# Performance work log

Hardware: AMD Instinct MI355X
Metric: run time of the kernel (lower is better)

## Reference

```python
import jax, jax.numpy as jnp
import numpy as np

NUM_EMBEDDINGS = 512
EMBEDDING_DIM = 64
COMMITMENT_SCALAR = 0.25


def setup_inputs() -> dict:
    key = jax.random.key(0)
    k_in, k_emb = jax.random.split(key)
    inputs = jax.random.normal(k_in, (64, 4096, EMBEDDING_DIM), dtype=jnp.float32)
    # nn.Embedding weight, init U(-1/K, 1/K) as in the torch module
    emb_weight = jax.random.uniform(
        k_emb, (NUM_EMBEDDINGS, EMBEDDING_DIM), dtype=jnp.float32,
        minval=-1.0 / NUM_EMBEDDINGS, maxval=1.0 / NUM_EMBEDDINGS)
    return {"inputs": inputs, "emb_weight": emb_weight}


def reference(inputs, emb_weight):
    input_shape = inputs.shape
    flat = inputs.reshape(-1, EMBEDDING_DIM)  # [N, D]
    distances = (jnp.sum(flat ** 2, axis=1, keepdims=True)
                 + jnp.sum(emb_weight ** 2, axis=1)
                 - 2.0 * flat @ emb_weight.T)
    encoding_indices = jnp.argmin(distances, axis=1)  # [N]
    # one-hot @ codebook == gather of codebook rows
    quantized = emb_weight[encoding_indices].reshape(input_shape)
    e_latent_loss = jnp.mean((jax.lax.stop_gradient(quantized) - inputs) ** 2)
    q_latent_loss = jnp.mean((quantized - jax.lax.stop_gradient(inputs)) ** 2)
    loss = q_latent_loss + COMMITMENT_SCALAR * e_latent_loss
    # straight-through estimator (training mode)
    quantized = inputs + jax.lax.stop_gradient(quantized - inputs)
    return encoding_indices[:, None], quantized, loss
```

## Files before the change

kernel.cpp:

```cpp
#include <hip/hip_runtime.h>


#define NROWS (64 * 4096)
#define DIMS 64
#define KCODES 512
#define BLOCK 256
#define GRID (NROWS / BLOCK)
#define WS_S2_OFF 0
#define WS_RED_OFF 4096

typedef unsigned int u16v __attribute__((ext_vector_type(16)));

__device__ __forceinline__ float pairwise64_sq(const float4* v) {
  float a[64];
  #pragma unroll
  for (int c = 0; c < 16; ++c) {
    a[4 * c + 0] = v[c].x * v[c].x;
    a[4 * c + 1] = v[c].y * v[c].y;
    a[4 * c + 2] = v[c].z * v[c].z;
    a[4 * c + 3] = v[c].w * v[c].w;
  }
  float r0 = a[0], r1 = a[1], r2 = a[2], r3 = a[3];
  float r4 = a[4], r5 = a[5], r6 = a[6], r7 = a[7];
  #pragma unroll
  for (int i = 8; i < 64; i += 8) {
    r0 += a[i + 0]; r1 += a[i + 1]; r2 += a[i + 2]; r3 += a[i + 3];
    r4 += a[i + 4]; r5 += a[i + 5]; r6 += a[i + 6]; r7 += a[i + 7];
  }
  return ((r0 + r1) + (r2 + r3)) + ((r4 + r5) + (r6 + r7));
}

__global__ void vq_s2(const float* __restrict__ emb, float* __restrict__ s2) {
  int k = blockIdx.x * 256 + threadIdx.x;
  const float4* row = (const float4*)(emb + (size_t)k * DIMS);
  float4 r[16];
  #pragma unroll
  for (int c = 0; c < 16; ++c) r[c] = row[c];
  s2[k] = pairwise64_sq(r);
}

#define FMA4(E, j0, c)                                        \
  acc = fmaf(xv[c].x, __uint_as_float(E[(j0) + 0]), acc);     \
  acc = fmaf(xv[c].y, __uint_as_float(E[(j0) + 1]), acc);     \
  acc = fmaf(xv[c].z, __uint_as_float(E[(j0) + 2]), acc);     \
  acc = fmaf(xv[c].w, __uint_as_float(E[(j0) + 3]), acc);

__global__ __launch_bounds__(BLOCK, 4) void vq_main(
    const float* __restrict__ x, const float* __restrict__ emb,
    const float* __restrict__ s2, float* __restrict__ out_idx,
    float* __restrict__ out_q, double* __restrict__ ws) {
  __shared__ int   kidx[BLOCK];
  __shared__ double red[BLOCK / 64];
  const int tid = threadIdx.x;
  const int row0 = blockIdx.x * BLOCK;
  const int r = row0 + tid;

  float4 xv[16];
  {
    const float4* p = (const float4*)(x + (size_t)r * DIMS);
    #pragma unroll
    for (int c = 0; c < 16; ++c) xv[c] = p[c];
  }
  const float s1 = pairwise64_sq(xv);

  float d1 = 3.4e38f;
  int kbest = 0;
  #pragma unroll 1
  for (int k = 0; k < KCODES; ++k) {
    const float* pe = emb + (size_t)k * DIMS;
    const float* ps = s2 + k;
    u16v e0, e1, e2, e3;
    unsigned int bku;
    asm volatile(
        "s_load_dwordx16 %0, %5, 0x0\n\t"
        "s_load_dwordx16 %1, %5, 0x40\n\t"
        "s_load_dwordx16 %2, %5, 0x80\n\t"
        "s_load_dwordx16 %3, %5, 0xc0\n\t"
        "s_load_dword    %4, %6, 0x0\n\t"
        "s_waitcnt lgkmcnt(0)"
        : "=&s"(e0), "=&s"(e1), "=&s"(e2), "=&s"(e3), "=&s"(bku)
        : "s"(pe), "s"(ps));

    float acc = 0.f;
    FMA4(e0,  0, 0)  FMA4(e0,  4, 1)  FMA4(e0,  8, 2)  FMA4(e0, 12, 3)
    FMA4(e1,  0, 4)  FMA4(e1,  4, 5)  FMA4(e1,  8, 6)  FMA4(e1, 12, 7)
    FMA4(e2,  0, 8)  FMA4(e2,  4, 9)  FMA4(e2,  8, 10) FMA4(e2, 12, 11)
    FMA4(e3,  0, 12) FMA4(e3,  4, 13) FMA4(e3,  8, 14) FMA4(e3, 12, 15)

    float S = s1 + __uint_as_float(bku);
    float d = fmaf(-2.0f, acc, S);
    if (d < d1) { d1 = d; kbest = k; }
  }

  out_idx[r] = (float)kbest;
  kidx[tid] = kbest;

  double lsum = (double)d1;
  #pragma unroll
  for (int off = 32; off > 0; off >>= 1) lsum += __shfl_down(lsum, off);
  if ((tid & 63) == 0) red[tid >> 6] = lsum;

  __syncthreads();

  if (tid == 0) {
    double s = 0.0;
    #pragma unroll
    for (int w = 0; w < BLOCK / 64; ++w) s += red[w];
    ws[blockIdx.x] = s;
  }

  const float4* emb4 = (const float4*)emb;
  float4* outq4 = (float4*)out_q;
  #pragma unroll
  for (int it = 0; it < 16; ++it) {
    int idx = it * BLOCK + tid;
    int rr = idx >> 4, c = idx & 15;
    float4 v = emb4[(size_t)kidx[rr] * 16 + c];
    outq4[(size_t)(row0 + rr) * 16 + c] = v;
  }
}

__global__ void vq_loss_finalize(const double* __restrict__ ws,
                                 float* __restrict__ out_loss) {
  double s = 0.0;
  for (int i = threadIdx.x; i < GRID; i += 64) s += ws[i];
  #pragma unroll
  for (int off = 32; off > 0; off >>= 1) s += __shfl_down(s, off);
  if (threadIdx.x == 0)
    *out_loss = (float)(1.25 * s / (double)((size_t)NROWS * DIMS));
}

extern "C" void kernel_launch(void* const* d_in, const int* in_sizes, int n_in,
                              void* d_out, int out_size, void* d_ws, size_t ws_size,
                              hipStream_t stream) {
  (void)in_sizes; (void)n_in; (void)out_size; (void)ws_size;
  const float* x   = (const float*)d_in[0];
  const float* emb = (const float*)d_in[1];
  float* out      = (float*)d_out;
  float* out_idx  = out;
  float* out_q    = out + NROWS;
  float* out_loss = out + NROWS + (size_t)NROWS * DIMS;
  float*  ws_s2  = (float*)((char*)d_ws + WS_S2_OFF);
  double* ws_red = (double*)((char*)d_ws + WS_RED_OFF);

  vq_s2<<<2, 256, 0, stream>>>(emb, ws_s2);
  vq_main<<<GRID, BLOCK, 0, stream>>>(x, emb, ws_s2, out_idx, out_q, ws_red);
  vq_loss_finalize<<<1, 64, 0, stream>>>(ws_red, out_loss);
}
```

Baseline: 318.3 us.

## Screen codes with bf16 MFMA then rescore candidates in fp32

Replaces the per-thread scalar fp32 scan over all 512 codes with a two-pass bf16 MFMA screen. The codebook is staged as swizzled bf16 in LDS. The first pass finds each row's approximate minimum distance. The second pass collects codes within a norm-scaled margin of that minimum into a small candidate list, and one thread per row rescores the candidates with exact fp32 dot products, falling back to a full 512-code scan on overflow. The aim is to move the dominant FMA work onto matrix cores. The costs are running the MFMA pass twice, LDS atomics, and possible mismatches if bf16 error exceeds the heuristic margin.

```diff
diff --git a/kernel.cpp b/kernel.cpp
--- a/kernel.cpp
+++ b/kernel.cpp
@@ -4,12 +4,16 @@
 #define NROWS (64 * 4096)
 #define DIMS 64
 #define KCODES 512
-#define BLOCK 256
-#define GRID (NROWS / BLOCK)
+#define BLOCK 512
+#define WAVES 8
+#define RPB 128
+#define GRID (NROWS / RPB)
+#define CANDMAX 16
 #define WS_S2_OFF 0
 #define WS_RED_OFF 4096
 
-typedef unsigned int u16v __attribute__((ext_vector_type(16)));
+typedef __attribute__((ext_vector_type(8))) __bf16 bf16x8;
+typedef __attribute__((ext_vector_type(4))) float f32x4;
 
 __device__ __forceinline__ float pairwise64_sq(const float4* v) {
   float a[64];
@@ -39,83 +43,190 @@
   s2[k] = pairwise64_sq(r);
 }
 
-#define FMA4(E, j0, c)                                        \
-  acc = fmaf(xv[c].x, __uint_as_float(E[(j0) + 0]), acc);     \
-  acc = fmaf(xv[c].y, __uint_as_float(E[(j0) + 1]), acc);     \
-  acc = fmaf(xv[c].z, __uint_as_float(E[(j0) + 2]), acc);     \
-  acc = fmaf(xv[c].w, __uint_as_float(E[(j0) + 3]), acc);
-
-__global__ __launch_bounds__(BLOCK, 4) void vq_main(
+__device__ __forceinline__ float vq_exact(const float4* __restrict__ xp,
+                                          const float* __restrict__ emb,
+                                          float s1v, float s2k, int k) {
+  const float4* ep = (const float4*)(emb + (size_t)k * DIMS);
+  float acc = 0.f;
+  #pragma unroll
+  for (int c = 0; c < 16; ++c) {
+    float4 e = ep[c], xc = xp[c];
+    acc = fmaf(xc.x, e.x, acc);
+    acc = fmaf(xc.y, e.y, acc);
+    acc = fmaf(xc.z, e.z, acc);
+    acc = fmaf(xc.w, e.w, acc);
+  }
+  float S = s1v + s2k;
+  return fmaf(-2.0f, acc, S);
+}
+
+struct LdsM {
+  unsigned int cb[KCODES * 32];
+  float s2[KCODES];
+  float s1[RPB];
+  float dmin[RPB];
+  float thr[RPB];
+  int   cnt[RPB];
+  int   cand[RPB][CANDMAX];
+  int   kidx[RPB];
+  double red[WAVES];
+};
+
+__global__ __launch_bounds__(BLOCK, 2) void vq_main(
     const float* __restrict__ x, const float* __restrict__ emb,
-    const float* __restrict__ s2, float* __restrict__ out_idx,
+    const float* __restrict__ s2g, float* __restrict__ out_idx,
     float* __restrict__ out_q, double* __restrict__ ws) {
-  __shared__ int   kidx[BLOCK];
-  __shared__ double red[BLOCK / 64];
+  __shared__ LdsM L;
   const int tid = threadIdx.x;
-  const int row0 = blockIdx.x * BLOCK;
-  const int r = row0 + tid;
-
-  float4 xv[16];
-  {
-    const float4* p = (const float4*)(x + (size_t)r * DIMS);
+  const int wid = tid >> 6, lane = tid & 63;
+  const int row0 = blockIdx.x * RPB;
+
+  #pragma unroll
+  for (int i = 0; i < 8; ++i) {
+    int c = tid + i * BLOCK;
+    int code = c >> 3, seg = c & 7;
+    const float4* ep = (const float4*)(emb + (size_t)code * DIMS + seg * 8);
+    float4 u = ep[0], v = ep[1];
+    bf16x8 h;
+    h[0] = (__bf16)u.x; h[1] = (__bf16)u.y; h[2] = (__bf16)u.z; h[3] = (__bf16)u.w;
+    h[4] = (__bf16)v.x; h[5] = (__bf16)v.y; h[6] = (__bf16)v.z; h[7] = (__bf16)v.w;
+    int boff = code * 128 + ((seg * 16) ^ ((code & 7) << 4));
+    *(bf16x8*)((char*)L.cb + boff) = h;
+  }
+  if (tid < KCODES) L.s2[tid] = s2g[tid];
+  if (tid < RPB) {
+    float4 xv[16];
+    const float4* p = (const float4*)(x + (size_t)(row0 + tid) * DIMS);
     #pragma unroll
     for (int c = 0; c < 16; ++c) xv[c] = p[c];
-  }
-  const float s1 = pairwise64_sq(xv);
-
-  float d1 = 3.4e38f;
-  int kbest = 0;
-  #pragma unroll 1
-  for (int k = 0; k < KCODES; ++k) {
-    const float* pe = emb + (size_t)k * DIMS;
-    const float* ps = s2 + k;
-    u16v e0, e1, e2, e3;
-    unsigned int bku;
-    asm volatile(
-        "s_load_dwordx16 %0, %5, 0x0\n\t"
-        "s_load_dwordx16 %1, %5, 0x40\n\t"
-        "s_load_dwordx16 %2, %5, 0x80\n\t"
-        "s_load_dwordx16 %3, %5, 0xc0\n\t"
-        "s_load_dword    %4, %6, 0x0\n\t"
-        "s_waitcnt lgkmcnt(0)"
-        : "=&s"(e0), "=&s"(e1), "=&s"(e2), "=&s"(e3), "=&s"(bku)
-        : "s"(pe), "s"(ps));
-
-    float acc = 0.f;
-    FMA4(e0,  0, 0)  FMA4(e0,  4, 1)  FMA4(e0,  8, 2)  FMA4(e0, 12, 3)
-    FMA4(e1,  0, 4)  FMA4(e1,  4, 5)  FMA4(e1,  8, 6)  FMA4(e1, 12, 7)
-    FMA4(e2,  0, 8)  FMA4(e2,  4, 9)  FMA4(e2,  8, 10) FMA4(e2, 12, 11)
-    FMA4(e3,  0, 12) FMA4(e3,  4, 13) FMA4(e3,  8, 14) FMA4(e3, 12, 15)
-
-    float S = s1 + __uint_as_float(bku);
-    float d = fmaf(-2.0f, acc, S);
-    if (d < d1) { d1 = d; kbest = k; }
-  }
-
-  out_idx[r] = (float)kbest;
-  kidx[tid] = kbest;
-
-  double lsum = (double)d1;
+    L.s1[tid] = pairwise64_sq(xv);
+  }
+  __syncthreads();
+
+  const int rowb = wid * 16 + ((lane >> 4) << 2);
+  const int arow = row0 + wid * 16 + (lane & 15);
+  const int kb = (lane >> 4) * 8;
+  bf16x8 a0, a1;
+  {
+    const float* xr = x + (size_t)arow * DIMS + kb;
+    float4 u0 = *(const float4*)(xr);
+    float4 u1 = *(const float4*)(xr + 4);
+    float4 v0 = *(const float4*)(xr + 32);
+    float4 v1 = *(const float4*)(xr + 36);
+    a0[0] = (__bf16)u0.x; a0[1] = (__bf16)u0.y; a0[2] = (__bf16)u0.z; a0[3] = (__bf16)u0.w;
+    a0[4] = (__bf16)u1.x; a0[5] = (__bf16)u1.y; a0[6] = (__bf16)u1.z; a0[7] = (__bf16)u1.w;
+    a1[0] = (__bf16)v0.x; a1[1] = (__bf16)v0.y; a1[2] = (__bf16)v0.z; a1[3] = (__bf16)v0.w;
+    a1[4] = (__bf16)v1.x; a1[5] = (__bf16)v1.y; a1[6] = (__bf16)v1.z; a1[7] = (__bf16)v1.w;
+  }
+  const float s10 = L.s1[rowb + 0], s11 = L.s1[rowb + 1];
+  const float s12 = L.s1[rowb + 2], s13 = L.s1[rowb + 3];
+  const int mycol = lane & 15;
+  const int segb = (lane >> 4) * 16;
+
+  float cm0 = 3.4e38f, cm1 = 3.4e38f, cm2 = 3.4e38f, cm3 = 3.4e38f;
+  #pragma unroll 2
+  for (int cc = 0; cc < 32; ++cc) {
+    int code = cc * 16 + mycol;
+    int swz = (code & 7) << 4;
+    char* rbp = (char*)L.cb + code * 128;
+    bf16x8 b0 = *(bf16x8*)(rbp + ((segb) ^ swz));
+    bf16x8 b1 = *(bf16x8*)(rbp + ((segb + 64) ^ swz));
+    f32x4 acc = {0.f, 0.f, 0.f, 0.f};
+    acc = __builtin_amdgcn_mfma_f32_16x16x32_bf16(a0, b0, acc, 0, 0, 0);
+    acc = __builtin_amdgcn_mfma_f32_16x16x32_bf16(a1, b1, acc, 0, 0, 0);
+    float s2c = L.s2[code];
+    float d0 = (s10 + s2c) - 2.f * acc[0];
+    float d1 = (s11 + s2c) - 2.f * acc[1];
+    float d2 = (s12 + s2c) - 2.f * acc[2];
+    float d3 = (s13 + s2c) - 2.f * acc[3];
+    cm0 = fminf(cm0, d0); cm1 = fminf(cm1, d1);
+    cm2 = fminf(cm2, d2); cm3 = fminf(cm3, d3);
+  }
+  #pragma unroll
+  for (int m = 1; m < 16; m <<= 1) {
+    cm0 = fminf(cm0, __shfl_xor(cm0, m));
+    cm1 = fminf(cm1, __shfl_xor(cm1, m));
+    cm2 = fminf(cm2, __shfl_xor(cm2, m));
+    cm3 = fminf(cm3, __shfl_xor(cm3, m));
+  }
+  if (mycol == 0) {
+    L.dmin[rowb + 0] = cm0; L.dmin[rowb + 1] = cm1;
+    L.dmin[rowb + 2] = cm2; L.dmin[rowb + 3] = cm3;
+  }
+  __syncthreads();
+  if (tid < RPB) {
+    L.thr[tid] = L.dmin[tid] + (1e-3f * sqrtf(L.s1[tid]) + 1e-4f);
+    L.cnt[tid] = 0;
+  }
+  __syncthreads();
+
+  const float t0 = L.thr[rowb + 0], t1 = L.thr[rowb + 1];
+  const float t2 = L.thr[rowb + 2], t3 = L.thr[rowb + 3];
+  #pragma unroll 2
+  for (int cc = 0; cc < 32; ++cc) {
+    int code = cc * 16 + mycol;
+    int swz = (code & 7) << 4;
+    char* rbp = (char*)L.cb + code * 128;
+    bf16x8 b0 = *(bf16x8*)(rbp + ((segb) ^ swz));
+    bf16x8 b1 = *(bf16x8*)(rbp + ((segb + 64) ^ swz));
+    f32x4 acc = {0.f, 0.f, 0.f, 0.f};
+    acc = __builtin_amdgcn_mfma_f32_16x16x32_bf16(a0, b0, acc, 0, 0, 0);
+    acc = __builtin_amdgcn_mfma_f32_16x16x32_bf16(a1, b1, acc, 0, 0, 0);
+    float s2c = L.s2[code];
+    float d0 = (s10 + s2c) - 2.f * acc[0];
+    float d1 = (s11 + s2c) - 2.f * acc[1];
+    float d2 = (s12 + s2c) - 2.f * acc[2];
+    float d3 = (s13 + s2c) - 2.f * acc[3];
+    if (d0 <= t0) { int p = atomicAdd(&L.cnt[rowb + 0], 1); if (p < CANDMAX) L.cand[rowb + 0][p] = code; }
+    if (d1 <= t1) { int p = atomicAdd(&L.cnt[rowb + 1], 1); if (p < CANDMAX) L.cand[rowb + 1][p] = code; }
+    if (d2 <= t2) { int p = atomicAdd(&L.cnt[rowb + 2], 1); if (p < CANDMAX) L.cand[rowb + 2][p] = code; }
+    if (d3 <= t3) { int p = atomicAdd(&L.cnt[rowb + 3], 1); if (p < CANDMAX) L.cand[rowb + 3][p] = code; }
+  }
+  __syncthreads();
+
+  double lsum = 0.0;
+  if (tid < RPB) {
+    const int grow = row0 + tid;
+    const float s1v = L.s1[tid];
+    const float4* xp = (const float4*)(x + (size_t)grow * DIMS);
+    float bestd = 3.4e38f;
+    int bestk = KCODES;
+    int n = L.cnt[tid];
+    if (n > CANDMAX) {
+      for (int k = 0; k < KCODES; ++k) {
+        float dv = vq_exact(xp, emb, s1v, L.s2[k], k);
+        if (dv < bestd) { bestd = dv; bestk = k; }
+      }
+    } else {
+      for (int i = 0; i < n; ++i) {
+        int k = L.cand[tid][i];
+        float dv = vq_exact(xp, emb, s1v, L.s2[k], k);
+        if (dv < bestd || (dv == bestd && k < bestk)) { bestd = dv; bestk = k; }
+      }
+    }
+    out_idx[grow] = (float)bestk;
+    L.kidx[tid] = bestk;
+    lsum = (double)bestd;
+  }
+
   #pragma unroll
   for (int off = 32; off > 0; off >>= 1) lsum += __shfl_down(lsum, off);
-  if ((tid & 63) == 0) red[tid >> 6] = lsum;
-
-  __syncthreads();
-
+  if (lane == 0) L.red[wid] = lsum;
+  __syncthreads();
   if (tid == 0) {
-    double s = 0.0;
+    double ssum = 0.0;
     #pragma unroll
-    for (int w = 0; w < BLOCK / 64; ++w) s += red[w];
-    ws[blockIdx.x] = s;
+    for (int w = 0; w < WAVES; ++w) ssum += L.red[w];
+    ws[blockIdx.x] = ssum;
   }
 
   const float4* emb4 = (const float4*)emb;
   float4* outq4 = (float4*)out_q;
   #pragma unroll
-  for (int it = 0; it < 16; ++it) {
+  for (int it = 0; it < 4; ++it) {
     int idx = it * BLOCK + tid;
     int rr = idx >> 4, c = idx & 15;
-    float4 v = emb4[(size_t)kidx[rr] * 16 + c];
+    float4 v = emb4[(size_t)L.kidx[rr] * 16 + c];
     outq4[(size_t)(row0 + rr) * 16 + c] = v;
   }
 }
```

New measurement: 491.8 us. 1.55x slower.
